# Performance work log

Measured on AMD Instinct MI355X. Metric: run time of the kernel, lower is better.

Reference implementation:

```python
import jax, jax.numpy as jnp
import numpy as np

B, T, C, H = 4, 2048, 1024, 16
D = C // H  # head dim = 64


def setup_inputs() -> dict:
    key = jax.random.key(0)
    ks = jax.random.split(key, 5)
    s = 1.0 / np.sqrt(C)
    return {
        "x": jax.random.normal(ks[0], (B, T, C), jnp.float32),
        "Wq": jax.random.normal(ks[1], (C, C), jnp.float32) * s,
        "bq": jnp.zeros((C,), jnp.float32),
        "Wk": jax.random.normal(ks[2], (C, C), jnp.float32) * s,
        "bk": jnp.zeros((C,), jnp.float32),
        "Wv": jax.random.normal(ks[3], (C, C), jnp.float32) * s,
        "bv": jnp.zeros((C,), jnp.float32),
        "Wp": jax.random.normal(ks[4], (C, C), jnp.float32) * s,
        "bp": jnp.zeros((C,), jnp.float32),
    }


def reference(x, Wq, bq, Wk, bk, Wv, bv, Wp, bp):
    # linear projections -> [B, H, T, D]
    def heads(t):
        return t.reshape(B, T, H, D).transpose(0, 2, 1, 3)
    q = heads(x @ Wq.T + bq)
    k = heads(x @ Wk.T + bk)
    v = heads(x @ Wv.T + bv)
    scale = 1.0 / np.sqrt(D)
    att = jnp.einsum("bhtd,bhsd->bhts", q, k) * scale  # [B,H,T,T]
    causal = jnp.tril(jnp.ones((T, T), bool))
    att = jnp.where(causal[None, None], att, -jnp.inf)
    att = jax.nn.softmax(att, axis=-1)
    y = jnp.einsum("bhts,bhsd->bhtd", att, v)  # [B,H,T,D]
    y = y.transpose(0, 2, 1, 3).reshape(B, T, C)
    return y @ Wp.T + bp
```

## Files before the change

### kernel.cpp

```cpp
#include <hip/hip_runtime.h>

typedef float f32x4 __attribute__((ext_vector_type(4)));
typedef float f32x16 __attribute__((ext_vector_type(16)));
typedef __bf16 bf16x8 __attribute__((ext_vector_type(8)));
typedef unsigned short u16x8 __attribute__((ext_vector_type(8)));
typedef unsigned int u32x4 __attribute__((ext_vector_type(4)));

#define SCQ 0.1803368801111183f

__device__ inline unsigned short f2bf(float f) {
  unsigned int u = __builtin_bit_cast(unsigned int, f);
  u += 0x7FFFu + ((u >> 16) & 1u);
  return (unsigned short)(u >> 16);
}

__device__ inline float fexp2(float x) {
#if __has_builtin(__builtin_amdgcn_exp2f)
  return __builtin_amdgcn_exp2f(x);
#else
  return exp2f(x);
#endif
}

__device__ inline unsigned int cvtpk_bf16(float a, float b) {
  unsigned int r;
  __asm__("v_cvt_pk_bf16_f32 %0, %1, %2" : "=v"(r) : "v"(a), "v"(b));
  return r;
}
__device__ inline void permswap32(unsigned int& a, unsigned int& b) {
  __asm__("v_permlane32_swap_b32 %0, %1" : "+v"(a), "+v"(b));
}

__device__ inline void gload_lds16(const unsigned short* g, unsigned short* l) {
  __builtin_amdgcn_global_load_lds(
      (const __attribute__((address_space(1))) unsigned int*)g,
      (__attribute__((address_space(3))) unsigned int*)l, 16, 0, 0);
}

__global__ void cvt_x(const float* __restrict__ in, unsigned short* __restrict__ out) {
  int i = (blockIdx.x * 256 + threadIdx.x) * 4;
  float4 f = *(const float4*)(in + i);
  ushort4 o;
  o.x = f2bf(f.x); o.y = f2bf(f.y); o.z = f2bf(f.z); o.w = f2bf(f.w);
  *(ushort4*)(out + i) = o;
}

__global__ void cvt_w(const float* __restrict__ a, const float* __restrict__ b,
                      const float* __restrict__ c, const float* __restrict__ d,
                      unsigned short* __restrict__ oa, unsigned short* __restrict__ ob,
                      unsigned short* __restrict__ oc, unsigned short* __restrict__ od) {
  const float* src[4] = {a, b, c, d};
  unsigned short* dst[4] = {oa, ob, oc, od};
  int m = blockIdx.y;
  int i = (blockIdx.x * 256 + threadIdx.x) * 4;
  float4 f = *(const float4*)(src[m] + i);
  ushort4 o;
  o.x = f2bf(f.x); o.y = f2bf(f.y); o.z = f2bf(f.z); o.w = f2bf(f.w);
  *(ushort4*)(dst[m] + i) = o;
}

template <int MODE>
__global__ __launch_bounds__(256) void gemm128(const unsigned short* __restrict__ A,
                                               const unsigned short* __restrict__ Bt,
                                               const float* __restrict__ b0,
                                               const float* __restrict__ b1,
                                               const float* __restrict__ b2,
                                               void* __restrict__ out,
                                               int M, int N, int K) {
  __shared__ __align__(16) unsigned short As[128 * 64];
  __shared__ __align__(16) unsigned short Bs[128 * 64];
  const int tid = threadIdx.x;
  const int lane = tid & 63, w = tid >> 6;
  const int l31 = lane & 31, half = lane >> 5;
  const int wm = w & 1, wn = w >> 1;
  const int m0 = blockIdx.x * 128, n0 = blockIdx.y * 128;

  f32x16 acc[2][2] = {};

  for (int kb = 0; kb < K; kb += 64) {
#pragma unroll
    for (int j = 0; j < 4; j++) {
      int ch = j * 256 + w * 64 + lane;
      int row = ch >> 3, pc = ch & 7;
      int c = pc ^ (row & 7);
      gload_lds16(A + (size_t)(m0 + row) * K + kb + c * 8, As + (size_t)(j * 256 + w * 64) * 8);
      gload_lds16(Bt + (size_t)(n0 + row) * K + kb + c * 8, Bs + (size_t)(j * 256 + w * 64) * 8);
    }
    __syncthreads();
#pragma unroll
    for (int ks = 0; ks < 64; ks += 16) {
      bf16x8 af[2], bfr[2];
#pragma unroll
      for (int at = 0; at < 2; at++) {
        int row = wm * 64 + at * 32 + l31;
        int pc = ((ks >> 3) + half) ^ (row & 7);
        af[at] = *(const bf16x8*)(As + row * 64 + pc * 8);
      }
#pragma unroll
      for (int nt = 0; nt < 2; nt++) {
        int row = wn * 64 + nt * 32 + l31;
        int pc = ((ks >> 3) + half) ^ (row & 7);
        bfr[nt] = *(const bf16x8*)(Bs + row * 64 + pc * 8);
      }
#pragma unroll
      for (int at = 0; at < 2; at++)
#pragma unroll
        for (int nt = 0; nt < 2; nt++)
          acc[at][nt] = __builtin_amdgcn_mfma_f32_32x32x16_bf16(af[at], bfr[nt], acc[at][nt], 0, 0, 0);
    }
    __syncthreads();
  }

#pragma unroll
  for (int at = 0; at < 2; at++)
#pragma unroll
    for (int nt = 0; nt < 2; nt++) {
      int col = n0 + wn * 64 + nt * 32 + l31;
      float bv, sc;
      int which = 0, cl = col;
      if (MODE == 0) {
        which = col >> 10; cl = col & 1023;
        const float* bp = (which == 0) ? b0 : ((which == 1) ? b1 : b2);
        bv = bp[cl];
        sc = (which == 0) ? SCQ : 1.f;
      } else {
        bv = b0[col]; sc = 1.f;
      }
#pragma unroll
      for (int reg = 0; reg < 16; reg++) {
        int row = m0 + wm * 64 + at * 32 + (reg & 3) + 8 * (reg >> 2) + 4 * half;
        float v = (acc[at][nt][reg] + bv) * sc;
        if (MODE == 0) {
          int h = cl >> 6, d = cl & 63;
          int b = row >> 11, t = row & 2047;
          ((unsigned short*)out)[(size_t)which * 8388608 +
                                 ((size_t)((b * 16 + h) * 2048 + t)) * 64 + d] = f2bf(v);
        } else {
          ((float*)out)[(size_t)row * N + col] = v;
        }
      }
    }
}

__global__ __launch_bounds__(256) void transpose_v(const unsigned short* __restrict__ V,
                                                   unsigned short* __restrict__ Vt) {
  constexpr int P = 66;
  __shared__ unsigned short L[64 * P];
  const int tid = threadIdx.x;
  const int bh = blockIdx.y;
  const int t0 = blockIdx.x * 64;
  const unsigned short* Vp = V + (size_t)bh * 2048 * 64;
  unsigned short* Op = Vt + (size_t)bh * 64 * 2048;
#pragma unroll
  for (int j = 0; j < 2; j++) {
    int r = (tid >> 3) + j * 32;
    int c = (tid & 7) * 8;
    u16x8 v = *(const u16x8*)(Vp + (size_t)(t0 + r) * 64 + c);
#pragma unroll
    for (int i = 0; i < 4; i++) {
      unsigned int pk = (unsigned int)v[2 * i] | ((unsigned int)v[2 * i + 1] << 16);
      *(unsigned int*)&L[r * P + c + 2 * i] = pk;
    }
  }
  __syncthreads();
#pragma unroll
  for (int j = 0; j < 2; j++) {
    int ch = j * 256 + tid;
    int d = ch >> 3, tc = (ch & 7) * 8;
    u16x8 o;
#pragma unroll
    for (int k = 0; k < 8; k++) o[k] = L[(tc + k) * P + d];
    *(u16x8*)(Op + (size_t)d * 2048 + t0 + tc) = o;
  }
}

__global__ __launch_bounds__(256, 2) void attn_kernel(const unsigned short* __restrict__ Q,
                                                      const unsigned short* __restrict__ Km,
                                                      const unsigned short* __restrict__ Vt,
                                                      unsigned short* __restrict__ Y) {
  constexpr int T = 2048, D = 64;
  __shared__ __align__(16) unsigned short Ks[2][64 * 64];
  __shared__ __align__(16) unsigned short Vs[2][64 * 64];
  const int tid = threadIdx.x;
  const int lane = tid & 63, w = tid >> 6;
  const int l31 = lane & 31, half = lane >> 5;
  const int bh = blockIdx.x;
  const int b = bh >> 4, h = bh & 15;
  const int p = blockIdx.y;
  const unsigned short* Qp = Q + (size_t)bh * T * D;
  const unsigned short* Kp = Km + (size_t)bh * T * D;
  const unsigned short* Vp = Vt + (size_t)bh * D * T;

  const int bch0 = (w * 2) * 64, bch1 = (w * 2 + 1) * 64;
  const int ch0 = bch0 + lane, ch1 = bch1 + lane;
  const int row0 = ch0 >> 3, c0 = (ch0 & 7) ^ (row0 & 7);
  const int row1 = ch1 >> 3, c1 = (ch1 & 7) ^ (row1 & 7);

  for (int phase = 0; phase < 2; ++phase) {
    const int jt = phase ? (63 - (p * 4 + w)) : (p * 4 + w);
    const int qt = jt * 32;
    const int nit = phase ? (32 - 2 * p) : (2 * p + 2);
    const int qg = qt + l31;

    bf16x8 aq[4];
#pragma unroll
    for (int kc = 0; kc < 4; kc++)
      aq[kc] = *(const bf16x8*)(Qp + (size_t)qg * D + kc * 16 + half * 8);
    __asm__ __volatile__("" :: "v"(__builtin_bit_cast(f32x4, aq[0])),
                              "v"(__builtin_bit_cast(f32x4, aq[1])),
                              "v"(__builtin_bit_cast(f32x4, aq[2])),
                              "v"(__builtin_bit_cast(f32x4, aq[3])));

    f32x16 o0 = {}, o1 = {};
    float lsum = 0.f;

    gload_lds16(Kp + (size_t)row0 * 64 + c0 * 8, Ks[0] + bch0 * 8);
    gload_lds16(Kp + (size_t)row1 * 64 + c1 * 8, Ks[0] + bch1 * 8);
    gload_lds16(Vp + (size_t)row0 * T + c0 * 8, Vs[0] + bch0 * 8);
    gload_lds16(Vp + (size_t)row1 * T + c1 * 8, Vs[0] + bch1 * 8);

    int cur = 0;
    for (int it = 0; it < nit; ++it) {
      const int s0 = it * 64;
      if (it + 1 < nit) {
        const int s1 = s0 + 64;
        unsigned short* kd = Ks[cur ^ 1];
        unsigned short* vd = Vs[cur ^ 1];
        gload_lds16(Kp + (size_t)(s1 + row0) * 64 + c0 * 8, kd + bch0 * 8);
        gload_lds16(Kp + (size_t)(s1 + row1) * 64 + c1 * 8, kd + bch1 * 8);
        gload_lds16(Vp + (size_t)row0 * T + s1 + c0 * 8, vd + bch0 * 8);
        gload_lds16(Vp + (size_t)row1 * T + s1 + c1 * 8, vd + bch1 * 8);
        __asm__ __volatile__("s_waitcnt vmcnt(4)" ::: "memory");
      } else {
        __asm__ __volatile__("s_waitcnt vmcnt(0)" ::: "memory");
      }
      __builtin_amdgcn_s_barrier();
      __builtin_amdgcn_sched_barrier(0);

      if (s0 <= qt + 31) {
        const unsigned short* Kb_ = Ks[cur];
        const unsigned short* Vb_ = Vs[cur];

        f32x16 sacc0 = {}, sacc1 = {};
#pragma unroll
        for (int kc = 0; kc < 4; kc++) {
          int kr0 = l31;
          int cc0 = (kc * 2 + half) ^ (kr0 & 7);
          u16x8 k0 = *(const u16x8*)(Kb_ + kr0 * 64 + cc0 * 8);
          sacc0 = __builtin_amdgcn_mfma_f32_32x32x16_bf16(
              __builtin_bit_cast(bf16x8, k0), aq[kc], sacc0, 0, 0, 0);
          int kr1 = 32 + l31;
          int cc1 = (kc * 2 + half) ^ (kr1 & 7);
          u16x8 k1 = *(const u16x8*)(Kb_ + kr1 * 64 + cc1 * 8);
          sacc1 = __builtin_amdgcn_mfma_f32_32x32x16_bf16(
              __builtin_bit_cast(bf16x8, k1), aq[kc], sacc1, 0, 0, 0);
        }

        const bool full = (s0 + 63) <= qt;
        float e0_[16], e1_[16];
        if (full) {
#pragma unroll
          for (int r = 0; r < 16; r++) { e0_[r] = fexp2(sacc0[r]); lsum += e0_[r]; }
#pragma unroll
          for (int r = 0; r < 16; r++) { e1_[r] = fexp2(sacc1[r]); lsum += e1_[r]; }
        } else {
#pragma unroll
          for (int r = 0; r < 16; r++) {
            int sg = s0 + (r & 3) + 8 * (r >> 2) + 4 * half;
            float ex = fexp2(sacc0[r]);
            ex = (sg > qg) ? 0.f : ex;
            e0_[r] = ex; lsum += ex;
          }
#pragma unroll
          for (int r = 0; r < 16; r++) {
            int sg = s0 + 32 + (r & 3) + 8 * (r >> 2) + 4 * half;
            float ex = fexp2(sacc1[r]);
            ex = (sg > qg) ? 0.f : ex;
            e1_[r] = ex; lsum += ex;
          }
        }

        bf16x8 pf[4];
        auto pack2 = [&](const float* e_, int kbase) {
#pragma unroll
          for (int kl = 0; kl < 2; kl++) {
            int base = kl * 8;
            unsigned int a0 = cvtpk_bf16(e_[base + 0], e_[base + 1]);
            unsigned int b0v = cvtpk_bf16(e_[base + 4], e_[base + 5]);
            permswap32(a0, b0v);
            unsigned int a1 = cvtpk_bf16(e_[base + 2], e_[base + 3]);
            unsigned int b1v = cvtpk_bf16(e_[base + 6], e_[base + 7]);
            permswap32(a1, b1v);
            u32x4 t = {a0, a1, b0v, b1v};
            pf[kbase + kl] = __builtin_bit_cast(bf16x8, t);
          }
        };
        pack2(e0_, 0);
        pack2(e1_, 2);

#pragma unroll
        for (int kc = 0; kc < 4; kc++) {
          int vr0 = l31;
          int cc0 = (kc * 2 + half) ^ (vr0 & 7);
          u16x8 v0 = *(const u16x8*)(Vb_ + vr0 * 64 + cc0 * 8);
          o0 = __builtin_amdgcn_mfma_f32_32x32x16_bf16(
              __builtin_bit_cast(bf16x8, v0), pf[kc], o0, 0, 0, 0);
          int vr1 = 32 + l31;
          int cc1 = (kc * 2 + half) ^ (vr1 & 7);
          u16x8 v1 = *(const u16x8*)(Vb_ + vr1 * 64 + cc1 * 8);
          o1 = __builtin_amdgcn_mfma_f32_32x32x16_bf16(
              __builtin_bit_cast(bf16x8, v1), pf[kc], o1, 0, 0, 0);
        }
      }

      __builtin_amdgcn_sched_barrier(0);
      __builtin_amdgcn_s_barrier();
      cur ^= 1;
    }

    float tot = lsum + __shfl_xor(lsum, 32);
    float inv = 1.f / tot;
    unsigned short* Yrow = Y + ((size_t)(b * T + qg)) * 1024 + h * 64;
#pragma unroll
    for (int rp = 0; rp < 8; rp++) {
      int r = rp * 2;
      int d = (r & 3) + 8 * (r >> 2) + 4 * half;
      *(unsigned int*)(Yrow + d)      = cvtpk_bf16(o0[r] * inv, o0[r + 1] * inv);
      *(unsigned int*)(Yrow + 32 + d) = cvtpk_bf16(o1[r] * inv, o1[r + 1] * inv);
    }
  }
}

extern "C" void kernel_launch(void* const* d_in, const int* in_sizes, int n_in,
                              void* d_out, int out_size, void* d_ws, size_t ws_size,
                              hipStream_t stream) {
  const float* x  = (const float*)d_in[0];
  const float* Wq = (const float*)d_in[1];
  const float* bq = (const float*)d_in[2];
  const float* Wk = (const float*)d_in[3];
  const float* bk = (const float*)d_in[4];
  const float* Wv = (const float*)d_in[5];
  const float* bv = (const float*)d_in[6];
  const float* Wp = (const float*)d_in[7];
  const float* bp = (const float*)d_in[8];

  char* ws = (char*)d_ws;
  unsigned short* xb  = (unsigned short*)(ws + 0);
  unsigned short* wqb = (unsigned short*)(ws + 16777216);
  unsigned short* wkb = (unsigned short*)(ws + 18874368);
  unsigned short* wvb = (unsigned short*)(ws + 20971520);
  unsigned short* wpb = (unsigned short*)(ws + 23068672);
  unsigned short* Qb  = (unsigned short*)(ws + 25165824);
  unsigned short* Kb  = (unsigned short*)(ws + 41943040);
  unsigned short* Vb  = (unsigned short*)(ws + 58720256);
  unsigned short* Vtb = xb;
  unsigned short* Yb  = Vb;

  cvt_x<<<8192, 256, 0, stream>>>(x, xb);
  cvt_w<<<dim3(1024, 4), 256, 0, stream>>>(Wq, Wk, Wv, Wp, wqb, wkb, wvb, wpb);

  gemm128<0><<<dim3(64, 24), 256, 0, stream>>>(xb, wqb, bq, bk, bv, Qb, 8192, 3072, 1024);

  transpose_v<<<dim3(32, 64), 256, 0, stream>>>(Vb, Vtb);
  attn_kernel<<<dim3(64, 8), 256, 0, stream>>>(Qb, Kb, Vtb, Yb);

  gemm128<1><<<dim3(64, 8), 256, 0, stream>>>(Yb, wpb, bp, bp, bp, d_out, 8192, 1024, 1024);
}
```

Before: 249.0 us.

## Replace 128x128 GEMM with pipelined 256x256 double-buffered GEMM with XCD-aware tile mapping

```diff
diff --git a/kernel.cpp b/kernel.cpp
--- a/kernel.cpp
+++ b/kernel.cpp
@@ -60,62 +60,144 @@
 }
 
 template <int MODE>
-__global__ __launch_bounds__(256) void gemm128(const unsigned short* __restrict__ A,
-                                               const unsigned short* __restrict__ Bt,
-                                               const float* __restrict__ b0,
-                                               const float* __restrict__ b1,
-                                               const float* __restrict__ b2,
-                                               void* __restrict__ out,
-                                               int M, int N, int K) {
-  __shared__ __align__(16) unsigned short As[128 * 64];
-  __shared__ __align__(16) unsigned short Bs[128 * 64];
+__global__ __launch_bounds__(512, 2) void gemm256(const unsigned short* __restrict__ A,
+                                                  const unsigned short* __restrict__ Bt,
+                                                  const float* __restrict__ b0,
+                                                  const float* __restrict__ b1,
+                                                  const float* __restrict__ b2,
+                                                  void* __restrict__ out,
+                                                  int M, int N, int K) {
+  __shared__ __align__(16) unsigned short Lg[2][4][128 * 64];
   const int tid = threadIdx.x;
   const int lane = tid & 63, w = tid >> 6;
-  const int l31 = lane & 31, half = lane >> 5;
-  const int wm = w & 1, wn = w >> 1;
-  const int m0 = blockIdx.x * 128, n0 = blockIdx.y * 128;
-
-  f32x16 acc[2][2] = {};
-
-  for (int kb = 0; kb < K; kb += 64) {
-#pragma unroll
-    for (int j = 0; j < 4; j++) {
-      int ch = j * 256 + w * 64 + lane;
-      int row = ch >> 3, pc = ch & 7;
-      int c = pc ^ (row & 7);
-      gload_lds16(A + (size_t)(m0 + row) * K + kb + c * 8, As + (size_t)(j * 256 + w * 64) * 8);
-      gload_lds16(Bt + (size_t)(n0 + row) * K + kb + c * 8, Bs + (size_t)(j * 256 + w * 64) * 8);
-    }
-    __syncthreads();
-#pragma unroll
-    for (int ks = 0; ks < 64; ks += 16) {
-      bf16x8 af[2], bfr[2];
-#pragma unroll
-      for (int at = 0; at < 2; at++) {
-        int row = wm * 64 + at * 32 + l31;
-        int pc = ((ks >> 3) + half) ^ (row & 7);
-        af[at] = *(const bf16x8*)(As + row * 64 + pc * 8);
-      }
-#pragma unroll
-      for (int nt = 0; nt < 2; nt++) {
-        int row = wn * 64 + nt * 32 + l31;
-        int pc = ((ks >> 3) + half) ^ (row & 7);
-        bfr[nt] = *(const bf16x8*)(Bs + row * 64 + pc * 8);
-      }
-#pragma unroll
-      for (int at = 0; at < 2; at++)
-#pragma unroll
-        for (int nt = 0; nt < 2; nt++)
-          acc[at][nt] = __builtin_amdgcn_mfma_f32_32x32x16_bf16(af[at], bfr[nt], acc[at][nt], 0, 0, 0);
-    }
-    __syncthreads();
+  const int qm = w >> 2, qn = w & 3;
+  const int l15 = lane & 15, kq = lane >> 4;
+
+  const int nwg = gridDim.x, qx = nwg >> 3;
+  const int wg = blockIdx.x;
+  const int wgs = (wg & 7) * qx + (wg >> 3);
+  const int nbm = M >> 8;
+  const int bm = wgs % nbm, bn = wgs / nbm;
+  const int m0 = bm * 256, n0 = bn * 256;
+  const int NT = K >> 6, NT4 = NT << 2;
+
+  const int row0 = tid >> 3, c0 = (tid & 7) ^ (row0 & 7);
+  const int row1 = row0 + 64, c1 = (tid & 7) ^ (row1 & 7);
+  const int ch0 = tid, ch1 = tid + 512;
+
+  auto stage = [&](int g) {
+    if (g < NT4) {
+      const int tt = g >> 2, h = g & 3;
+      const unsigned short* s_;
+      int rbase, reg_;
+      if (h == 0)      { s_ = A;  rbase = m0;       reg_ = 0; }
+      else if (h == 3) { s_ = A;  rbase = m0 + 128; reg_ = 1; }
+      else if (h == 1) { s_ = Bt; rbase = n0;       reg_ = 2; }
+      else             { s_ = Bt; rbase = n0 + 128; reg_ = 3; }
+      unsigned short* d = &Lg[tt & 1][reg_][0];
+      gload_lds16(s_ + (size_t)(rbase + row0) * K + tt * 64 + c0 * 8, d + ch0 * 8);
+      gload_lds16(s_ + (size_t)(rbase + row1) * K + tt * 64 + c1 * 8, d + ch1 * 8);
+    }
+  };
+
+  auto rdAh = [&](const unsigned short* R, u16x8 (&a)[4][2]) {
+#pragma unroll
+    for (int mf = 0; mf < 4; mf++) {
+      int row = qm * 64 + mf * 16 + l15;
+#pragma unroll
+      for (int kf = 0; kf < 2; kf++) {
+        int pc = (kf * 4 + kq) ^ (row & 7);
+        a[mf][kf] = *(const u16x8*)(R + row * 64 + pc * 8);
+      }
+    }
+  };
+  auto rdBh = [&](const unsigned short* R, u16x8 (&bb)[2][2]) {
+#pragma unroll
+    for (int nf = 0; nf < 2; nf++) {
+      int row = qn * 32 + nf * 16 + l15;
+#pragma unroll
+      for (int kf = 0; kf < 2; kf++) {
+        int pc = (kf * 4 + kq) ^ (row & 7);
+        bb[nf][kf] = *(const u16x8*)(R + row * 64 + pc * 8);
+      }
+    }
+  };
+  auto domfma = [&](u16x8 (&a)[4][2], u16x8 (&bb)[2][2], f32x4 (*ac)[2]) {
+#pragma unroll
+    for (int mf = 0; mf < 4; mf++)
+#pragma unroll
+      for (int nf = 0; nf < 2; nf++)
+#pragma unroll
+        for (int kf = 0; kf < 2; kf++)
+          ac[mf][nf] = __builtin_amdgcn_mfma_f32_16x16x32_bf16(
+              __builtin_bit_cast(bf16x8, a[mf][kf]),
+              __builtin_bit_cast(bf16x8, bb[nf][kf]), ac[mf][nf], 0, 0, 0);
+  };
+
+  f32x4 acc[4][4][2] = {};
+
+#pragma unroll
+  for (int g = 0; g < 7; ++g) stage(g);
+  __asm__ __volatile__("s_waitcnt vmcnt(6)" ::: "memory");
+  __builtin_amdgcn_s_barrier();
+
+  for (int tt = 0; tt < NT; ++tt) {
+    const unsigned short* A0r = &Lg[tt & 1][0][0];
+    const unsigned short* A1r = &Lg[tt & 1][1][0];
+    const unsigned short* B0r = &Lg[tt & 1][2][0];
+    const unsigned short* B1r = &Lg[tt & 1][3][0];
+    const int gb = 7 + 4 * tt;
+    u16x8 aA[4][2], bb0[2][2], bb1[2][2];
+
+    rdAh(A0r, aA); rdBh(B0r, bb0);
+    stage(gb + 0);
+    __builtin_amdgcn_s_barrier();
+    __asm__ __volatile__("s_waitcnt lgkmcnt(0)" ::: "memory");
+    __builtin_amdgcn_sched_barrier(0);
+    __builtin_amdgcn_s_setprio(1);
+    domfma(aA, bb0, acc[0]);
+    __builtin_amdgcn_s_setprio(0);
+    __builtin_amdgcn_s_barrier();
+
+    rdBh(B1r, bb1);
+    stage(gb + 1);
+    __builtin_amdgcn_s_barrier();
+    __asm__ __volatile__("s_waitcnt lgkmcnt(0)" ::: "memory");
+    __builtin_amdgcn_sched_barrier(0);
+    __builtin_amdgcn_s_setprio(1);
+    domfma(aA, bb1, acc[1]);
+    __builtin_amdgcn_s_setprio(0);
+    __builtin_amdgcn_s_barrier();
+
+    rdAh(A1r, aA);
+    stage(gb + 2);
+    __builtin_amdgcn_s_barrier();
+    __asm__ __volatile__("s_waitcnt lgkmcnt(0)" ::: "memory");
+    __builtin_amdgcn_sched_barrier(0);
+    __builtin_amdgcn_s_setprio(1);
+    domfma(aA, bb0, acc[2]);
+    __builtin_amdgcn_s_setprio(0);
+    __builtin_amdgcn_s_barrier();
+
+    stage(gb + 3);
+    __builtin_amdgcn_s_setprio(1);
+    domfma(aA, bb1, acc[3]);
+    __builtin_amdgcn_s_setprio(0);
+    if (tt < NT - 2) {
+      __asm__ __volatile__("s_waitcnt vmcnt(6)" ::: "memory");
+    } else if (tt == NT - 2) {
+      __asm__ __volatile__("s_waitcnt vmcnt(0)" ::: "memory");
+    }
+    __builtin_amdgcn_s_barrier();
   }
 
 #pragma unroll
-  for (int at = 0; at < 2; at++)
-#pragma unroll
-    for (int nt = 0; nt < 2; nt++) {
-      int col = n0 + wn * 64 + nt * 32 + l31;
+  for (int p = 0; p < 4; p++) {
+    const int rb = m0 + (p >> 1) * 128 + qm * 64 + kq * 4;
+    const int cb = n0 + (p & 1) * 128 + qn * 32 + l15;
+#pragma unroll
+    for (int nf = 0; nf < 2; nf++) {
+      const int col = cb + nf * 16;
       float bv, sc;
       int which = 0, cl = col;
       if (MODE == 0) {
@@ -127,19 +209,24 @@
         bv = b0[col]; sc = 1.f;
       }
 #pragma unroll
-      for (int reg = 0; reg < 16; reg++) {
-        int row = m0 + wm * 64 + at * 32 + (reg & 3) + 8 * (reg >> 2) + 4 * half;
-        float v = (acc[at][nt][reg] + bv) * sc;
-        if (MODE == 0) {
-          int h = cl >> 6, d = cl & 63;
-          int b = row >> 11, t = row & 2047;
-          ((unsigned short*)out)[(size_t)which * 8388608 +
-                                 ((size_t)((b * 16 + h) * 2048 + t)) * 64 + d] = f2bf(v);
-        } else {
-          ((float*)out)[(size_t)row * N + col] = v;
+      for (int mf = 0; mf < 4; mf++) {
+        f32x4 v4 = acc[p][mf][nf];
+#pragma unroll
+        for (int r = 0; r < 4; r++) {
+          int row = rb + mf * 16 + r;
+          float v = (v4[r] + bv) * sc;
+          if (MODE == 0) {
+            int h = cl >> 6, d = cl & 63;
+            int b = row >> 11, t = row & 2047;
+            ((unsigned short*)out)[(size_t)which * 8388608 +
+                                   ((size_t)((b * 16 + h) * 2048 + t)) * 64 + d] = f2bf(v);
+          } else {
+            ((float*)out)[(size_t)row * N + col] = v;
+          }
         }
       }
     }
+  }
 }
 
 __global__ __launch_bounds__(256) void transpose_v(const unsigned short* __restrict__ V,
@@ -359,10 +446,10 @@
   cvt_x<<<8192, 256, 0, stream>>>(x, xb);
   cvt_w<<<dim3(1024, 4), 256, 0, stream>>>(Wq, Wk, Wv, Wp, wqb, wkb, wvb, wpb);
 
-  gemm128<0><<<dim3(64, 24), 256, 0, stream>>>(xb, wqb, bq, bk, bv, Qb, 8192, 3072, 1024);
+  gemm256<0><<<384, 512, 0, stream>>>(xb, wqb, bq, bk, bv, Qb, 8192, 3072, 1024);
 
   transpose_v<<<dim3(32, 64), 256, 0, stream>>>(Vb, Vtb);
   attn_kernel<<<dim3(64, 8), 256, 0, stream>>>(Qb, Kb, Vtb, Yb);
 
-  gemm128<1><<<dim3(64, 8), 256, 0, stream>>>(Yb, wpb, bp, bp, bp, d_out, 8192, 1024, 1024);
-}
+  gemm256<1><<<128, 512, 0, stream>>>(Yb, wpb, bp, bp, bp, d_out, 8192, 1024, 1024);
+}
```

New measurement: 265.5 us. +6.6%, slower.
